# Kernel optimization log

Hardware: AMD Instinct MI355X
Metric: run time of the kernel (lower is better)

## Reference

```python
import jax, jax.numpy as jnp
import numpy as np

N_NODES = 50000
N_EDGES = 800000
H = 128
CHEM_DIM = 34   # 2 + 2*num_gdf
GEOM_DIM = 48   # 2*num_gdf + num_signatures
EPS = 1e-5


def _linear_params(key, d_in, d_out):
    kw, kb = jax.random.split(key)
    lim = 1.0 / np.sqrt(d_in)
    w = jax.random.uniform(kw, (d_in, d_out), jnp.float32, -lim, lim)
    b = jax.random.uniform(kb, (d_out,), jnp.float32, -lim, lim)
    return w, b


def setup_inputs() -> dict:
    key = jax.random.key(0)
    ks = jax.random.split(key, 16)
    inp = {
        'chem_feats': jax.random.normal(ks[0], (N_EDGES, CHEM_DIM), jnp.float32),
        'geom_feats': jax.random.normal(ks[1], (N_NODES, GEOM_DIM), jnp.float32),
        'nbr_vids': jax.random.randint(ks[2], (N_EDGES,), 0, N_NODES, jnp.int32),
    }
    # chem_mlp: Linear(34,128) -> BN(128) -> SiLU -> Linear(128,256) -> BN(256)
    inp['w_c1'], inp['b_c1'] = _linear_params(ks[3], CHEM_DIM, H)
    inp['g_c1'], inp['be_c1'] = jnp.ones((H,), jnp.float32), jnp.zeros((H,), jnp.float32)
    inp['w_c2'], inp['b_c2'] = _linear_params(ks[4], H, 2 * H)
    inp['g_c2'], inp['be_c2'] = jnp.ones((2 * H,), jnp.float32), jnp.zeros((2 * H,), jnp.float32)
    # geom_mlp: Linear(48,64) -> BN(64) -> SiLU -> Linear(64,64) -> BN(64)
    inp['w_g1'], inp['b_g1'] = _linear_params(ks[5], GEOM_DIM, H // 2)
    inp['g_g1'], inp['be_g1'] = jnp.ones((H // 2,), jnp.float32), jnp.zeros((H // 2,), jnp.float32)
    inp['w_g2'], inp['b_g2'] = _linear_params(ks[6], H // 2, H // 2)
    inp['g_g2'], inp['be_g2'] = jnp.ones((H // 2,), jnp.float32), jnp.zeros((H // 2,), jnp.float32)
    # feat_mlp: Linear(192,128) -> BN(128) -> SiLU -> Linear(128,128) -> BN(128)
    inp['w_f1'], inp['b_f1'] = _linear_params(ks[7], H + H // 2, H)
    inp['g_f1'], inp['be_f1'] = jnp.ones((H,), jnp.float32), jnp.zeros((H,), jnp.float32)
    inp['w_f2'], inp['b_f2'] = _linear_params(ks[8], H, H)
    inp['g_f2'], inp['be_f2'] = jnp.ones((H,), jnp.float32), jnp.zeros((H,), jnp.float32)
    return inp


def _bn(x, gamma, beta):
    # BatchNorm1d with batch statistics (training-mode normalization; dropout = identity at eval)
    m = jnp.mean(x, axis=0)
    v = jnp.var(x, axis=0)
    return gamma * (x - m) * jax.lax.rsqrt(v + EPS) + beta


def reference(chem_feats, geom_feats, nbr_vids,
              w_c1, b_c1, g_c1, be_c1, w_c2, b_c2, g_c2, be_c2,
              w_g1, b_g1, g_g1, be_g1, w_g2, b_g2, g_g2, be_g2,
              w_f1, b_f1, g_f1, be_f1, w_f2, b_f2, g_f2, be_f2):
    # chem branch: per-edge MLP
    h = _bn(chem_feats @ w_c1 + b_c1, g_c1, be_c1)
    h = jax.nn.silu(h)
    h = _bn(h @ w_c2 + b_c2, g_c2, be_c2)            # [E, 2H]
    nbr_filter, nbr_core = jnp.split(h, 2, axis=-1)
    h_chem = jax.nn.sigmoid(nbr_filter) * jax.nn.softplus(nbr_core)  # [E, H]
    # scatter-sum per-edge features into node bins
    h_chem = jax.ops.segment_sum(h_chem, nbr_vids, num_segments=N_NODES)  # [N, H]
    # geom branch: per-node MLP
    hg = _bn(geom_feats @ w_g1 + b_g1, g_g1, be_g1)
    hg = jax.nn.silu(hg)
    h_geom = _bn(hg @ w_g2 + b_g2, g_g2, be_g2)      # [N, H/2]
    # fuse
    hf = jnp.concatenate((h_chem, h_geom), axis=-1)  # [N, 3H/2]
    hf = _bn(hf @ w_f1 + b_f1, g_f1, be_f1)
    hf = jax.nn.silu(hf)
    h_out = _bn(hf @ w_f2 + b_f2, g_f2, be_f2)       # [N, H]
    return h_out
```

## Files before the change

### kernel.cpp

```cpp
#include <hip/hip_runtime.h>
#include <hip/hip_bf16.h>
#include <cmath>

#define E_EDGES 800000
#define N_NODES 50000
#define BN_EPS 1e-5f

typedef __attribute__((ext_vector_type(8))) short short8;
typedef __attribute__((ext_vector_type(4))) float float4v;
typedef unsigned short ushort_t;

#define MFMA16(a, b, c) __builtin_amdgcn_mfma_f32_16x16x32_bf16((a), (b), (c), 0, 0, 0)

#define OFF_GX 0
#define OFF_GH 2304
#define OFF_A1 23040
#define OFF_C1 23168
#define OFF_A2 23296
#define OFF_C2 23552
#define OFF_GS1SUM 23808
#define OFF_GS1SQ 23872
#define OFF_GS2SUM 23936
#define OFF_GS2SQ 24000
#define OFF_FS1SUM 24064
#define OFF_FS1SQ 24192
#define OFF_FS2SUM 24320
#define OFF_FS2SQ 24448
#define OFF_NODE 24576
#define OFF_TG2 (OFF_NODE + N_NODES * 128)
#define OFF_TF1 (OFF_TG2 + N_NODES * 64)
#define OFF_TF2 OFF_NODE
#define OFF_W1T (OFF_TF1 + N_NODES * 128)
#define OFF_W2T (OFF_W1T + 4096)

__device__ __forceinline__ float frcp_(float x) { return __builtin_amdgcn_rcpf(x); }
__device__ __forceinline__ float sigmoid_(float x) { return frcp_(1.0f + __expf(-x)); }
__device__ __forceinline__ float softplus_(float x) {
  return (x > 20.0f) ? x : __logf(1.0f + __expf(x));
}
__device__ __forceinline__ float silu_(float x) { return x * frcp_(1.0f + __expf(-x)); }

__device__ __forceinline__ ushort_t f2bf(float f) {
  __hip_bfloat16 h = __float2bfloat16(f);
  return *(ushort_t*)&h;
}
__device__ __forceinline__ float bf2f(ushort_t u) {
  return __uint_as_float(((unsigned)u) << 16);
}

__device__ __forceinline__ void load_xfrag(const float* __restrict__ chem, int e, int qd,
                                           short8* x0, short8* x1) {
  const float* xe = chem + e * 34;
  float2 p0 = *(const float2*)(xe + 8 * qd);
  float2 p1 = *(const float2*)(xe + 8 * qd + 2);
  float2 p2 = *(const float2*)(xe + 8 * qd + 4);
  float2 p3 = *(const float2*)(xe + 8 * qd + 6);
  short8 a;
  a[0] = (short)f2bf(p0.x); a[1] = (short)f2bf(p0.y);
  a[2] = (short)f2bf(p1.x); a[3] = (short)f2bf(p1.y);
  a[4] = (short)f2bf(p2.x); a[5] = (short)f2bf(p2.y);
  a[6] = (short)f2bf(p3.x); a[7] = (short)f2bf(p3.y);
  *x0 = a;
  short8 b = (short8){0, 0, 0, 0, 0, 0, 0, 0};
  if (qd == 0) {
    float2 pt = *(const float2*)(xe + 32);
    b[0] = (short)f2bf(pt.x); b[1] = (short)f2bf(pt.y);
  }
  *x1 = b;
}

__global__ __launch_bounds__(256) void k_prep(const float* __restrict__ w1,
                                              const float* __restrict__ w2,
                                              float* __restrict__ ws) {
  ushort_t* w1t = (ushort_t*)(ws + OFF_W1T);
  ushort_t* w2t = (ushort_t*)(ws + OFF_W2T);
  int idx = blockIdx.x * 256 + threadIdx.x;
  if (idx < 128 * 64) {
    int c = idx >> 6, k = idx & 63;
    float v = (k < 34) ? w1[k * 128 + c] : 0.0f;
    w1t[idx] = f2bf(v);
  }
  int j = idx - 128 * 64;
  if (j >= 0 && j < 256 * 128) {
    int c = j >> 7, k = j & 127;
    w2t[j] = f2bf(w2[k * 256 + c]);
  }
}

__global__ __launch_bounds__(256) void k_xstats(const float* __restrict__ chem,
                                                float* __restrict__ ws) {
  __shared__ __align__(16) ushort_t xT[2][48 * 72];
  const int t = threadIdx.x, wv = t >> 6, ln = t & 63, r15 = ln & 15, qd = ln >> 4;
  for (int i = t; i < 2 * 14 * 72; i += 256) {
    int b = i / (14 * 72), j = i % (14 * 72);
    int rr = j / 72, e = j % 72;
    xT[b][(34 + rr) * 72 + e] = (rr == 0 && e < 64) ? f2bf(1.0f) : (ushort_t)0;
  }
  float4v g0 = {0, 0, 0, 0}, g1 = {0, 0, 0, 0};
#pragma unroll 2
  for (int it = 0; it < 10; ++it) {
    const int st = blockIdx.x * 10 + it;
    const int buf = it & 1;
    for (int i = t; i < 64 * 34; i += 256) {
      int e = i / 34, k = i - e * 34;
      xT[buf][k * 72 + e] = f2bf(chem[st * 2176 + i]);
    }
    __syncthreads();
    const ushort_t* xb = &xT[buf][0];
#pragma unroll
    for (int ks = 0; ks < 2; ++ks) {
      const ushort_t* xk = xb + ks * 32 + 8 * qd;
      short8 f0 = *(const short8*)&xk[(0 + r15) * 72];
      short8 f1 = *(const short8*)&xk[(16 + r15) * 72];
      short8 f2v = *(const short8*)&xk[(32 + r15) * 72];
      if (wv == 0) { g0 = MFMA16(f0, f0, g0); g1 = MFMA16(f0, f1, g1); }
      else if (wv == 1) { g0 = MFMA16(f0, f2v, g0); g1 = MFMA16(f1, f1, g1); }
      else if (wv == 2) { g0 = MFMA16(f1, f2v, g0); }
      else { g0 = MFMA16(f2v, f2v, g0); }
    }
  }
  float* GX = ws + OFF_GX;
  int ti0, tj0, ti1 = -1, tj1 = -1;
  if (wv == 0) { ti0 = 0; tj0 = 0; ti1 = 0; tj1 = 1; }
  else if (wv == 1) { ti0 = 0; tj0 = 2; ti1 = 1; tj1 = 1; }
  else if (wv == 2) { ti0 = 1; tj0 = 2; }
  else { ti0 = 2; tj0 = 2; }
#pragma unroll
  for (int r = 0; r < 4; ++r)
    atomicAdd(&GX[(16 * ti0 + 4 * qd + r) * 48 + 16 * tj0 + r15], g0[r]);
  if (ti1 >= 0)
#pragma unroll
    for (int r = 0; r < 4; ++r)
      atomicAdd(&GX[(16 * ti1 + 4 * qd + r) * 48 + 16 * tj1 + r15], g1[r]);
}

__global__ __launch_bounds__(64) void k_bn1(const float* __restrict__ b1,
                                            const float* __restrict__ g1,
                                            const float* __restrict__ be1,
                                            float* __restrict__ ws) {
  const int c = blockIdx.x, i = threadIdx.x;
  __shared__ float wc[34];
  const ushort_t* w1t = (const ushort_t*)(ws + OFF_W1T);
  const float* GX = ws + OFF_GX;
  if (i < 34) wc[i] = bf2f(w1t[c * 64 + i]);
  __syncthreads();
  float p = 0.0f, ps = 0.0f;
  if (i < 34) {
    float gi = 0.0f;
    for (int j = 0; j < 34; ++j) {
      int a = i, b = j;
      if ((a >> 4) > (b >> 4)) { int tt = a; a = b; b = tt; }
      gi += GX[a * 48 + b] * wc[j];
    }
    p = wc[i] * gi;
    ps = wc[i] * GX[i * 48 + 34];
  }
#pragma unroll
  for (int off = 1; off < 64; off <<= 1) {
    p += __shfl_xor(p, off);
    ps += __shfl_xor(ps, off);
  }
  if (i == 0) {
    const float E = (float)E_EDGES;
    float bc = b1[c];
    float sum = ps + E * bc;
    float sq = p + 2.0f * bc * ps + E * bc * bc;
    float m = sum / E, v = sq / E - m * m;
    float a = g1[c] * rsqrtf(v + BN_EPS);
    ws[OFF_A1 + c] = a;
    ws[OFF_C1 + c] = a * (bc - m) + be1[c];
  }
}

template <int TJA, int TJB>
__device__ __forceinline__ void ghstep(const ushort_t* hk, int r15, float4v (&g)[11]) {
  short8 f[TJB + 1];
#pragma unroll
  for (int i = 0; i <= TJB; ++i) f[i] = *(const short8*)&hk[(16 * i + r15) * 72];
  short8 f8 = *(const short8*)&hk[(128 + r15) * 72];
  int s = 0;
#pragma unroll
  for (int ti = 0; ti <= TJA; ++ti) { g[s] = MFMA16(f[ti], f[TJA], g[s]); ++s; }
  g[s] = MFMA16(f8, f[TJA], g[s]); ++s;
#pragma unroll
  for (int ti = 0; ti <= TJB; ++ti) { g[s] = MFMA16(f[ti], f[TJB], g[s]); ++s; }
  g[s] = MFMA16(f8, f[TJB], g[s]);
}

__device__ __forceinline__ void ghtile(float* GH, int ti, int tj, int r15, int qd,
                                       const float4v v) {
#pragma unroll
  for (int r = 0; r < 4; ++r)
    atomicAdd(&GH[(16 * ti + 4 * qd + r) * 144 + 16 * tj + r15], v[r]);
}

template <int TJA, int TJB>
__device__ __forceinline__ void ghflush(float* GH, int r15, int qd, const float4v (&g)[11]) {
  int s = 0;
#pragma unroll
  for (int ti = 0; ti <= TJA; ++ti) { ghtile(GH, ti, TJA, r15, qd, g[s]); ++s; }
  ghtile(GH, 8, TJA, r15, qd, g[s]); ++s;
#pragma unroll
  for (int ti = 0; ti <= TJB; ++ti) { ghtile(GH, ti, TJB, r15, qd, g[s]); ++s; }
  ghtile(GH, 8, TJB, r15, qd, g[s]);
}

__global__ __launch_bounds__(256) void k_h(const float* __restrict__ chem,
                                           float* __restrict__ ws) {
  __shared__ __align__(16) ushort_t hT[2][144 * 72];
  const int t = threadIdx.x, wv = t >> 6, ln = t & 63, r15 = ln & 15, qd = ln >> 4;
  const ushort_t* w1t = (const ushort_t*)(ws + OFF_W1T);
  for (int i = t; i < 2 * 16 * 72; i += 256) {
    int b = i / (16 * 72), j = i % (16 * 72);
    int rr = j / 72, e = j % 72;
    hT[b][(128 + rr) * 72 + e] = (rr == 0 && e < 64) ? f2bf(1.0f) : (ushort_t)0;
  }
  float a1c[2], c1c[2];
#pragma unroll
  for (int cf = 0; cf < 2; ++cf) {
    int col = 32 * wv + 16 * cf + r15;
    a1c[cf] = ws[OFF_A1 + col];
    c1c[cf] = ws[OFF_C1 + col];
  }
  float4v gacc[11];
#pragma unroll
  for (int s = 0; s < 11; ++s) gacc[s] = (float4v){0, 0, 0, 0};

#pragma unroll 2
  for (int it = 0; it < 10; ++it) {
    const int st = blockIdx.x * 10 + it;
    const int buf = it & 1;
    const int e_base = st * 64;
    short8 xa0[4], xa1[4];
#pragma unroll
    for (int rb = 0; rb < 4; ++rb)
      load_xfrag(chem, e_base + 16 * rb + r15, qd, &xa0[rb], &xa1[rb]);
#pragma unroll
    for (int cf = 0; cf < 2; ++cf) {
      const int col = 32 * wv + 16 * cf + r15;
      short8 wb0 = *(const short8*)&w1t[col * 64 + 8 * qd];
      short8 wb1 = *(const short8*)&w1t[col * 64 + 32 + 8 * qd];
#pragma unroll
      for (int rb = 0; rb < 4; ++rb) {
        float4v acc = (float4v){0, 0, 0, 0};
        acc = MFMA16(xa0[rb], wb0, acc);
        acc = MFMA16(xa1[rb], wb1, acc);
        unsigned long long pk = 0;
#pragma unroll
        for (int r = 0; r < 4; ++r) {
          float hv = silu_(fmaf(a1c[cf], acc[r], c1c[cf]));
          pk |= ((unsigned long long)f2bf(hv)) << (16 * r);
        }
        *(unsigned long long*)&hT[buf][col * 72 + 16 * rb + 4 * qd] = pk;
      }
    }
    __syncthreads();
    const ushort_t* hb = &hT[buf][0];
#pragma unroll
    for (int ks = 0; ks < 2; ++ks) {
      const ushort_t* hk = hb + ks * 32 + 8 * qd;
      if (wv == 0) ghstep<0, 7>(hk, r15, gacc);
      else if (wv == 1) ghstep<1, 6>(hk, r15, gacc);
      else if (wv == 2) ghstep<2, 5>(hk, r15, gacc);
      else ghstep<3, 4>(hk, r15, gacc);
    }
  }
  float* GH = ws + OFF_GH;
  if (wv == 0) ghflush<0, 7>(GH, r15, qd, gacc);
  else if (wv == 1) ghflush<1, 6>(GH, r15, qd, gacc);
  else if (wv == 2) ghflush<2, 5>(GH, r15, qd, gacc);
  else ghflush<3, 4>(GH, r15, qd, gacc);
}

__global__ __launch_bounds__(128) void k_bn2(const float* __restrict__ b2,
                                             const float* __restrict__ g2,
                                             const float* __restrict__ be2,
                                             float* __restrict__ ws) {
  const int c = blockIdx.x, i = threadIdx.x;
  __shared__ float wcol[128];
  __shared__ float redQ[2], redS[2];
  const ushort_t* w2t = (const ushort_t*)(ws + OFF_W2T);
  const float* GH = ws + OFF_GH;
  wcol[i] = bf2f(w2t[c * 128 + i]);
  __syncthreads();
  float wi = wcol[i];
  float gi = 0.0f;
  for (int j = 0; j < 128; ++j) {
    int a = i, b = j;
    if ((a >> 4) > (b >> 4)) { int tt = a; a = b; b = tt; }
    gi += GH[a * 144 + b] * wcol[j];
  }
  float p = wi * gi;
  float ps = wi * GH[128 * 144 + i];
#pragma unroll
  for (int off = 1; off < 64; off <<= 1) {
    p += __shfl_xor(p, off);
    ps += __shfl_xor(ps, off);
  }
  const int wv = i >> 6, ln = i & 63;
  if (ln == 0) { redQ[wv] = p; redS[wv] = ps; }
  __syncthreads();
  if (i == 0) {
    float q = redQ[0] + redQ[1], s = redS[0] + redS[1];
    const float E = (float)E_EDGES;
    float bc = b2[c];
    float sum = s + E * bc;
    float sq = q + 2.0f * bc * s + E * bc * bc;
    float m = sum / E, v = sq / E - m * m;
    float a = g2[c] * rsqrtf(v + BN_EPS);
    ws[OFF_A2 + c] = a;
    ws[OFF_C2 + c] = a * (bc - m) + be2[c];
  }
}

__global__ __launch_bounds__(256) void k_scatter(const float* __restrict__ chem,
                                                 const int* __restrict__ vids,
                                                 float* __restrict__ ws) {
  __shared__ __align__(16) ushort_t hS[2][64 * 136];
  const int t = threadIdx.x, wv = t >> 6, ln = t & 63, r15 = ln & 15, qd = ln >> 4;
  const ushort_t* w1t = (const ushort_t*)(ws + OFF_W1T);
  const ushort_t* w2t = (const ushort_t*)(ws + OFF_W2T);
  float* node = ws + OFF_NODE;
  float a1c[2], c1c[2], aF2[2], cF2[2], aC2[2], cC2[2];
#pragma unroll
  for (int cf = 0; cf < 2; ++cf) {
    int col = 32 * wv + 16 * cf + r15;
    a1c[cf] = ws[OFF_A1 + col];
    c1c[cf] = ws[OFF_C1 + col];
    aF2[cf] = ws[OFF_A2 + col];
    cF2[cf] = ws[OFF_C2 + col];
    aC2[cf] = ws[OFF_A2 + 128 + col];
    cC2[cf] = ws[OFF_C2 + 128 + col];
  }
#pragma unroll 2
  for (int it = 0; it < 8; ++it) {
    const int st = blockIdx.x * 8 + it;
    if (st >= 12500) break;
    const int buf = it & 1;
    const int e_base = st * 64;
    const int myvid = vids[e_base + ln];
    short8 xa0[4], xa1[4];
#pragma unroll
    for (int rb = 0; rb < 4; ++rb)
      load_xfrag(chem, e_base + 16 * rb + r15, qd, &xa0[rb], &xa1[rb]);
#pragma unroll
    for (int cf = 0; cf < 2; ++cf) {
      const int col = 32 * wv + 16 * cf + r15;
      short8 wb0 = *(const short8*)&w1t[col * 64 + 8 * qd];
      short8 wb1 = *(const short8*)&w1t[col * 64 + 32 + 8 * qd];
#pragma unroll
      for (int rb = 0; rb < 4; ++rb) {
        float4v acc = (float4v){0, 0, 0, 0};
        acc = MFMA16(xa0[rb], wb0, acc);
        acc = MFMA16(xa1[rb], wb1, acc);
#pragma unroll
        for (int r = 0; r < 4; ++r) {
          float hv = silu_(fmaf(a1c[cf], acc[r], c1c[cf]));
          hS[buf][(16 * rb + 4 * qd + r) * 136 + col] = f2bf(hv);
        }
      }
    }
    __syncthreads();
    const ushort_t* hb = &hS[buf][0];
#pragma unroll
    for (int cf = 0; cf < 2; ++cf) {
      const int colF = 32 * wv + 16 * cf + r15;
      float4v accF[4], accC[4];
#pragma unroll
      for (int rb = 0; rb < 4; ++rb) {
        accF[rb] = (float4v){0, 0, 0, 0};
        accC[rb] = (float4v){0, 0, 0, 0};
      }
#pragma unroll
      for (int ks = 0; ks < 4; ++ks) {
        short8 bF = *(const short8*)&w2t[colF * 128 + ks * 32 + 8 * qd];
        short8 bC = *(const short8*)&w2t[(128 + colF) * 128 + ks * 32 + 8 * qd];
#pragma unroll
        for (int rb = 0; rb < 4; ++rb) {
          short8 hf = *(const short8*)&hb[(16 * rb + r15) * 136 + ks * 32 + 8 * qd];
          accF[rb] = MFMA16(hf, bF, accF[rb]);
          accC[rb] = MFMA16(hf, bC, accC[rb]);
        }
      }
#pragma unroll
      for (int rb = 0; rb < 4; ++rb)
#pragma unroll
        for (int r = 0; r < 4; ++r) {
          float F = fmaf(aF2[cf], accF[rb][r], cF2[cf]);
          float Co = fmaf(aC2[cf], accC[rb][r], cC2[cf]);
          float gv = sigmoid_(F) * softplus_(Co);
          int vid = __shfl(myvid, 16 * rb + 4 * qd + r);
          atomicAdd(node + (size_t)vid * 128 + colF, gv);
        }
    }
  }
}

__global__ __launch_bounds__(256) void k_geom_stats1(const float* __restrict__ geom,
                                                     const float* __restrict__ wg1,
                                                     const float* __restrict__ bg1,
                                                     float* __restrict__ ws) {
  __shared__ float ssum[64], ssq[64];
  const int t = threadIdx.x, lane = t & 63, w = t >> 6;
  if (t < 64) { ssum[t] = 0.0f; ssq[t] = 0.0f; }
  __syncthreads();
  const float bcol = bg1[lane];
  const int nb = blockIdx.x * 16 + w * 4;
  float x[4], acc[4];
#pragma unroll
  for (int u = 0; u < 4; u++) {
    x[u] = (lane < 48) ? geom[(nb + u) * 48 + lane] : 0.0f;
    acc[u] = bcol;
  }
#pragma unroll 16
  for (int k = 0; k < 48; k++) {
    float wvv = wg1[k * 64 + lane];
#pragma unroll
    for (int u = 0; u < 4; u++) acc[u] = fmaf(__shfl(x[u], k), wvv, acc[u]);
  }
  float bs = 0.0f, bq = 0.0f;
#pragma unroll
  for (int u = 0; u < 4; u++) { bs += acc[u]; bq += acc[u] * acc[u]; }
  atomicAdd(&ssum[lane], bs);
  atomicAdd(&ssq[lane], bq);
  __syncthreads();
  if (t < 64) {
    atomicAdd(ws + OFF_GS1SUM + t, ssum[t]);
    atomicAdd(ws + OFF_GS1SQ + t, ssq[t]);
  }
}

__global__ __launch_bounds__(256) void k_geom_main(
    const float* __restrict__ geom, const float* __restrict__ wg1,
    const float* __restrict__ bg1, const float* __restrict__ gg1,
    const float* __restrict__ beg1, const float* __restrict__ wg2,
    const float* __restrict__ bg2, float* __restrict__ ws) {
  __shared__ float ssum[64], ssq[64];
  const int t = threadIdx.x, lane = t & 63, w = t >> 6;
  if (t < 64) { ssum[t] = 0.0f; ssq[t] = 0.0f; }
  const float invN = 1.0f / (float)N_NODES;
  float s1 = ws[OFF_GS1SUM + lane], q1 = ws[OFF_GS1SQ + lane];
  float m1 = s1 * invN, v1 = q1 * invN - m1 * m1;
  float a1 = gg1[lane] * rsqrtf(v1 + BN_EPS);
  float c1 = beg1[lane] - a1 * m1;
  const float bcol = bg1[lane], b2col = bg2[lane];
  __syncthreads();
  const int nb = blockIdx.x * 16 + w * 4;
  float x[4], tg1[4], hg[4], acc[4];
#pragma unroll
  for (int u = 0; u < 4; u++) {
    x[u] = (lane < 48) ? geom[(nb + u) * 48 + lane] : 0.0f;
    tg1[u] = bcol;
  }
#pragma unroll 16
  for (int k = 0; k < 48; k++) {
    float wvv = wg1[k * 64 + lane];
#pragma unroll
    for (int u = 0; u < 4; u++) tg1[u] = fmaf(__shfl(x[u], k), wvv, tg1[u]);
  }
#pragma unroll
  for (int u = 0; u < 4; u++) {
    hg[u] = silu_(fmaf(a1, tg1[u], c1));
    acc[u] = b2col;
  }
#pragma unroll 16
  for (int k = 0; k < 64; k++) {
    float wvv = wg2[k * 64 + lane];
#pragma unroll
    for (int u = 0; u < 4; u++) acc[u] = fmaf(__shfl(hg[u], k), wvv, acc[u]);
  }
  float bs = 0.0f, bq = 0.0f;
#pragma unroll
  for (int u = 0; u < 4; u++) {
    ws[OFF_TG2 + (nb + u) * 64 + lane] = acc[u];
    bs += acc[u]; bq += acc[u] * acc[u];
  }
  atomicAdd(&ssum[lane], bs);
  atomicAdd(&ssq[lane], bq);
  __syncthreads();
  if (t < 64) {
    atomicAdd(ws + OFF_GS2SUM + t, ssum[t]);
    atomicAdd(ws + OFF_GS2SQ + t, ssq[t]);
  }
}

__global__ __launch_bounds__(256) void k_fuse1(const float* __restrict__ wf1,
                                               const float* __restrict__ bf1,
                                               const float* __restrict__ gg2,
                                               const float* __restrict__ beg2,
                                               float* __restrict__ ws) {
  __shared__ float ssum[128], ssq[128];
  const int t = threadIdx.x, lane = t & 63, w = t >> 6;
  if (t < 128) { ssum[t] = 0.0f; ssq[t] = 0.0f; }
  const float invN = 1.0f / (float)N_NODES;
  float s2 = ws[OFF_GS2SUM + lane], q2 = ws[OFF_GS2SQ + lane];
  float mg = s2 * invN, vg = q2 * invN - mg * mg;
  float ag = gg2[lane] * rsqrtf(vg + BN_EPS);
  float cg_ = beg2[lane] - ag * mg;
  const float bA = bf1[lane], bB = bf1[64 + lane];
  __syncthreads();
  const int nb = blockIdx.x * 16 + w * 4;
  float xa[4], xb[4], xg[4], acc1[4], acc2[4];
#pragma unroll
  for (int u = 0; u < 4; u++) {
    int n = nb + u;
    xa[u] = ws[OFF_NODE + n * 128 + lane];
    xb[u] = ws[OFF_NODE + n * 128 + 64 + lane];
    xg[u] = fmaf(ag, ws[OFF_TG2 + n * 64 + lane], cg_);
    acc1[u] = bA; acc2[u] = bB;
  }
#pragma unroll 16
  for (int k = 0; k < 64; k++) {
    float w1v = wf1[k * 128 + lane], w2v = wf1[k * 128 + 64 + lane];
#pragma unroll
    for (int u = 0; u < 4; u++) {
      float xk = __shfl(xa[u], k);
      acc1[u] = fmaf(xk, w1v, acc1[u]);
      acc2[u] = fmaf(xk, w2v, acc2[u]);
    }
  }
#pragma unroll 16
  for (int k = 0; k < 64; k++) {
    float w1v = wf1[(64 + k) * 128 + lane], w2v = wf1[(64 + k) * 128 + 64 + lane];
#pragma unroll
    for (int u = 0; u < 4; u++) {
      float xk = __shfl(xb[u], k);
      acc1[u] = fmaf(xk, w1v, acc1[u]);
      acc2[u] = fmaf(xk, w2v, acc2[u]);
    }
  }
#pragma unroll 16
  for (int k = 0; k < 64; k++) {
    float w1v = wf1[(128 + k) * 128 + lane], w2v = wf1[(128 + k) * 128 + 64 + lane];
#pragma unroll
    for (int u = 0; u < 4; u++) {
      float xk = __shfl(xg[u], k);
      acc1[u] = fmaf(xk, w1v, acc1[u]);
      acc2[u] = fmaf(xk, w2v, acc2[u]);
    }
  }
  float sA = 0, qA = 0, sB = 0, qB = 0;
#pragma unroll
  for (int u = 0; u < 4; u++) {
    int n = nb + u;
    ws[OFF_TF1 + n * 128 + lane] = acc1[u];
    ws[OFF_TF1 + n * 128 + 64 + lane] = acc2[u];
    sA += acc1[u]; qA += acc1[u] * acc1[u];
    sB += acc2[u]; qB += acc2[u] * acc2[u];
  }
  atomicAdd(&ssum[lane], sA); atomicAdd(&ssq[lane], qA);
  atomicAdd(&ssum[64 + lane], sB); atomicAdd(&ssq[64 + lane], qB);
  __syncthreads();
  if (t < 128) {
    atomicAdd(ws + OFF_FS1SUM + t, ssum[t]);
    atomicAdd(ws + OFF_FS1SQ + t, ssq[t]);
  }
}

__global__ __launch_bounds__(256) void k_fuse2(const float* __restrict__ wf2,
                                               const float* __restrict__ bf2,
                                               const float* __restrict__ gf1,
                                               const float* __restrict__ bef1,
                                               float* __restrict__ ws) {
  __shared__ float ssum[128], ssq[128];
  const int t = threadIdx.x, lane = t & 63, w = t >> 6;
  if (t < 128) { ssum[t] = 0.0f; ssq[t] = 0.0f; }
  const float invN = 1.0f / (float)N_NODES;
  float sA_ = ws[OFF_FS1SUM + lane], qA_ = ws[OFF_FS1SQ + lane];
  float mA = sA_ * invN, vA = qA_ * invN - mA * mA;
  float aA = gf1[lane] * rsqrtf(vA + BN_EPS);
  float cA = bef1[lane] - aA * mA;
  float sB_ = ws[OFF_FS1SUM + 64 + lane], qB_ = ws[OFF_FS1SQ + 64 + lane];
  float mB = sB_ * invN, vB = qB_ * invN - mB * mB;
  float aB = gf1[64 + lane] * rsqrtf(vB + BN_EPS);
  float cB = bef1[64 + lane] - aB * mB;
  const float b1c = bf2[lane], b2c = bf2[64 + lane];
  __syncthreads();
  const int nb = blockIdx.x * 16 + w * 4;
  float ha[4], hb[4], acc1[4], acc2[4];
#pragma unroll
  for (int u = 0; u < 4; u++) {
    int n = nb + u;
    ha[u] = silu_(fmaf(aA, ws[OFF_TF1 + n * 128 + lane], cA));
    hb[u] = silu_(fmaf(aB, ws[OFF_TF1 + n * 128 + 64 + lane], cB));
    acc1[u] = b1c; acc2[u] = b2c;
  }
#pragma unroll 16
  for (int k = 0; k < 64; k++) {
    float w1v = wf2[k * 128 + lane], w2v = wf2[k * 128 + 64 + lane];
#pragma unroll
    for (int u = 0; u < 4; u++) {
      float xk = __shfl(ha[u], k);
      acc1[u] = fmaf(xk, w1v, acc1[u]);
      acc2[u] = fmaf(xk, w2v, acc2[u]);
    }
  }
#pragma unroll 16
  for (int k = 0; k < 64; k++) {
    float w1v = wf2[(64 + k) * 128 + lane], w2v = wf2[(64 + k) * 128 + 64 + lane];
#pragma unroll
    for (int u = 0; u < 4; u++) {
      float xk = __shfl(hb[u], k);
      acc1[u] = fmaf(xk, w1v, acc1[u]);
      acc2[u] = fmaf(xk, w2v, acc2[u]);
    }
  }
  float sA = 0, qA = 0, sB = 0, qB = 0;
#pragma unroll
  for (int u = 0; u < 4; u++) {
    int n = nb + u;
    ws[OFF_TF2 + n * 128 + lane] = acc1[u];
    ws[OFF_TF2 + n * 128 + 64 + lane] = acc2[u];
    sA += acc1[u]; qA += acc1[u] * acc1[u];
    sB += acc2[u]; qB += acc2[u] * acc2[u];
  }
  atomicAdd(&ssum[lane], sA); atomicAdd(&ssq[lane], qA);
  atomicAdd(&ssum[64 + lane], sB); atomicAdd(&ssq[64 + lane], qB);
  __syncthreads();
  if (t < 128) {
    atomicAdd(ws + OFF_FS2SUM + t, ssum[t]);
    atomicAdd(ws + OFF_FS2SQ + t, ssq[t]);
  }
}

__global__ __launch_bounds__(256) void k_final(const float* __restrict__ gf2,
                                               const float* __restrict__ bef2,
                                               const float* __restrict__ ws,
                                               float* __restrict__ out) {
  const int idx = blockIdx.x * 256 + threadIdx.x;
  const int base = idx * 4;
  if (base >= N_NODES * 128) return;
  const float invN = 1.0f / (float)N_NODES;
  const int c0 = base & 127;
  float4 v = *(const float4*)(ws + OFF_TF2 + base);
  float vv[4] = {v.x, v.y, v.z, v.w}, r[4];
#pragma unroll
  for (int j = 0; j < 4; j++) {
    int c = c0 + j;
    float s = ws[OFF_FS2SUM + c], q = ws[OFF_FS2SQ + c];
    float m = s * invN, var = q * invN - m * m;
    float a = gf2[c] * rsqrtf(var + BN_EPS);
    r[j] = fmaf(a, vv[j] - m, bef2[c]);
  }
  *(float4*)(out + base) = make_float4(r[0], r[1], r[2], r[3]);
}

extern "C" void kernel_launch(void* const* d_in, const int* in_sizes, int n_in,
                              void* d_out, int out_size, void* d_ws, size_t ws_size,
                              hipStream_t stream) {
  const float* chem = (const float*)d_in[0];
  const float* geom = (const float*)d_in[1];
  const int* vids = (const int*)d_in[2];
  const float* w_c1 = (const float*)d_in[3];  const float* b_c1 = (const float*)d_in[4];
  const float* g_c1 = (const float*)d_in[5];  const float* be_c1 = (const float*)d_in[6];
  const float* w_c2 = (const float*)d_in[7];  const float* b_c2 = (const float*)d_in[8];
  const float* g_c2 = (const float*)d_in[9];  const float* be_c2 = (const float*)d_in[10];
  const float* w_g1 = (const float*)d_in[11]; const float* b_g1 = (const float*)d_in[12];
  const float* g_g1 = (const float*)d_in[13]; const float* be_g1 = (const float*)d_in[14];
  const float* w_g2 = (const float*)d_in[15]; const float* b_g2 = (const float*)d_in[16];
  const float* g_g2 = (const float*)d_in[17]; const float* be_g2 = (const float*)d_in[18];
  const float* w_f1 = (const float*)d_in[19]; const float* b_f1 = (const float*)d_in[20];
  const float* g_f1 = (const float*)d_in[21]; const float* be_f1 = (const float*)d_in[22];
  const float* w_f2 = (const float*)d_in[23]; const float* b_f2 = (const float*)d_in[24];
  const float* g_f2 = (const float*)d_in[25]; const float* be_f2 = (const float*)d_in[26];
  float* ws = (float*)d_ws;
  float* out = (float*)d_out;

  hipMemsetAsync(d_ws, 0, (size_t)(OFF_NODE + N_NODES * 128) * sizeof(float), stream);

  k_prep<<<dim3(160), dim3(256), 0, stream>>>(w_c1, w_c2, ws);
  k_xstats<<<dim3(1250), dim3(256), 0, stream>>>(chem, ws);
  k_bn1<<<dim3(128), dim3(64), 0, stream>>>(b_c1, g_c1, be_c1, ws);
  k_h<<<dim3(1250), dim3(256), 0, stream>>>(chem, ws);
  k_bn2<<<dim3(256), dim3(128), 0, stream>>>(b_c2, g_c2, be_c2, ws);
  k_scatter<<<dim3(1563), dim3(256), 0, stream>>>(chem, vids, ws);
  k_geom_stats1<<<dim3(3125), dim3(256), 0, stream>>>(geom, w_g1, b_g1, ws);
  k_geom_main<<<dim3(3125), dim3(256), 0, stream>>>(geom, w_g1, b_g1, g_g1, be_g1, w_g2, b_g2, ws);
  k_fuse1<<<dim3(3125), dim3(256), 0, stream>>>(w_f1, b_f1, g_g2, be_g2, ws);
  k_fuse2<<<dim3(3125), dim3(256), 0, stream>>>(w_f2, b_f2, g_f1, be_f1, ws);
  k_final<<<dim3(6250), dim3(256), 0, stream>>>(g_f2, be_f2, ws, out);
}
```

Before: 1.195 ms.

## Sort edges by node via counting sort and segment-reduce before atomics

Adds a histogram, two-level prefix scan and fill pass that build a node-sorted edge permutation. The scatter kernel then gathers chem rows in that order and stages the gated outputs in shared memory. It run-length reduces consecutive equal node ids before each atomicAdd, aiming to cut the roughly 100M float atomics. In exchange it adds four small kernels with their own int atomics, an indirect row gather, an extra barrier, and drops the double-buffered shared tile. With about 16 edges per node, each 32-row half-tile run should collapse many atomics.

Result: no change. 1.173 ms (-1.9%).

```diff
diff --git a/kernel.cpp b/kernel.cpp
--- a/kernel.cpp
+++ b/kernel.cpp
@@ -32,6 +32,12 @@
 #define OFF_TF2 OFF_NODE
 #define OFF_W1T (OFF_TF1 + N_NODES * 128)
 #define OFF_W2T (OFF_W1T + 4096)
+#define OFF_BASEI (OFF_W2T + 16384)
+#define OFF_BTOT (OFF_BASEI + 50176)
+#define OFF_CNT (OFF_BTOT + 256)
+#define OFF_CUR (OFF_CNT + 50176)
+#define OFF_SIDX (OFF_CUR + 50176)
+#define OFF_VIDS (OFF_SIDX + E_EDGES)
 
 __device__ __forceinline__ float frcp_(float x) { return __builtin_amdgcn_rcpf(x); }
 __device__ __forceinline__ float sigmoid_(float x) { return frcp_(1.0f + __expf(-x)); }
@@ -87,6 +93,74 @@
   }
 }
 
+__global__ __launch_bounds__(256) void k_hist(const int* __restrict__ vids,
+                                              float* __restrict__ ws) {
+  const int e = blockIdx.x * 256 + threadIdx.x;
+  int* cnt = (int*)(ws + OFF_CNT);
+  if (e < E_EDGES) atomicAdd(&cnt[vids[e]], 1);
+}
+
+__global__ __launch_bounds__(256) void k_scan1(float* __restrict__ ws) {
+  const int* cnt = (const int*)(ws + OFF_CNT);
+  int* base = (int*)(ws + OFF_BASEI);
+  int* btot = (int*)(ws + OFF_BTOT);
+  const int t = threadIdx.x, b = blockIdx.x, i = b * 256 + t;
+  const int lane = t & 63, w = t >> 6;
+  int c = (i < N_NODES) ? cnt[i] : 0;
+  int s = c;
+#pragma unroll
+  for (int o = 1; o < 64; o <<= 1) {
+    int y = __shfl_up(s, o);
+    if (lane >= o) s += y;
+  }
+  __shared__ int wsum[4];
+  if (lane == 63) wsum[w] = s;
+  __syncthreads();
+  int add = 0;
+#pragma unroll
+  for (int k = 0; k < 4; ++k)
+    if (k < w) add += wsum[k];
+  base[i] = s + add - c;
+  if (t == 255) btot[b] = s + add;
+}
+
+__global__ __launch_bounds__(256) void k_scan2(float* __restrict__ ws) {
+  int* btot = (int*)(ws + OFF_BTOT);
+  const int t = threadIdx.x;
+  const int lane = t & 63, w = t >> 6;
+  int c = (t < 196) ? btot[t] : 0;
+  int s = c;
+#pragma unroll
+  for (int o = 1; o < 64; o <<= 1) {
+    int y = __shfl_up(s, o);
+    if (lane >= o) s += y;
+  }
+  __shared__ int wsum[4];
+  if (lane == 63) wsum[w] = s;
+  __syncthreads();
+  int add = 0;
+#pragma unroll
+  for (int k = 0; k < 4; ++k)
+    if (k < w) add += wsum[k];
+  if (t < 196) btot[t] = s + add - c;
+}
+
+__global__ __launch_bounds__(256) void k_fill(const int* __restrict__ vids,
+                                              float* __restrict__ ws) {
+  const int e = blockIdx.x * 256 + threadIdx.x;
+  const int* base = (const int*)(ws + OFF_BASEI);
+  const int* btot = (const int*)(ws + OFF_BTOT);
+  int* cur = (int*)(ws + OFF_CUR);
+  int* sidx = (int*)(ws + OFF_SIDX);
+  int* vsrt = (int*)(ws + OFF_VIDS);
+  if (e < E_EDGES) {
+    int v = vids[e];
+    int pos = base[v] + btot[v >> 8] + atomicAdd(&cur[v], 1);
+    sidx[pos] = e;
+    vsrt[pos] = v;
+  }
+}
+
 __global__ __launch_bounds__(256) void k_xstats(const float* __restrict__ chem,
                                                 float* __restrict__ ws) {
   __shared__ __align__(16) ushort_t xT[2][48 * 72];
@@ -314,12 +388,15 @@
 }
 
 __global__ __launch_bounds__(256) void k_scatter(const float* __restrict__ chem,
-                                                 const int* __restrict__ vids,
                                                  float* __restrict__ ws) {
-  __shared__ __align__(16) ushort_t hS[2][64 * 136];
+  __shared__ __align__(16) ushort_t hS[64 * 136];
+  __shared__ __align__(16) float gS[64 * 133];
+  __shared__ int vS[64];
   const int t = threadIdx.x, wv = t >> 6, ln = t & 63, r15 = ln & 15, qd = ln >> 4;
   const ushort_t* w1t = (const ushort_t*)(ws + OFF_W1T);
   const ushort_t* w2t = (const ushort_t*)(ws + OFF_W2T);
+  const int* sidx = (const int*)(ws + OFF_SIDX);
+  const int* vsrt = (const int*)(ws + OFF_VIDS);
   float* node = ws + OFF_NODE;
   float a1c[2], c1c[2], aF2[2], cF2[2], aC2[2], cC2[2];
 #pragma unroll
@@ -332,17 +409,18 @@
     aC2[cf] = ws[OFF_A2 + 128 + col];
     cC2[cf] = ws[OFF_C2 + 128 + col];
   }
-#pragma unroll 2
   for (int it = 0; it < 8; ++it) {
     const int st = blockIdx.x * 8 + it;
     if (st >= 12500) break;
-    const int buf = it & 1;
     const int e_base = st * 64;
-    const int myvid = vids[e_base + ln];
+    const int myeid = sidx[e_base + ln];
+    const int myvid = vsrt[e_base + ln];
     short8 xa0[4], xa1[4];
 #pragma unroll
-    for (int rb = 0; rb < 4; ++rb)
-      load_xfrag(chem, e_base + 16 * rb + r15, qd, &xa0[rb], &xa1[rb]);
+    for (int rb = 0; rb < 4; ++rb) {
+      int er = __shfl(myeid, 16 * rb + r15);
+      load_xfrag(chem, er, qd, &xa0[rb], &xa1[rb]);
+    }
 #pragma unroll
     for (int cf = 0; cf < 2; ++cf) {
       const int col = 32 * wv + 16 * cf + r15;
@@ -356,12 +434,12 @@
 #pragma unroll
         for (int r = 0; r < 4; ++r) {
           float hv = silu_(fmaf(a1c[cf], acc[r], c1c[cf]));
-          hS[buf][(16 * rb + 4 * qd + r) * 136 + col] = f2bf(hv);
+          hS[(16 * rb + 4 * qd + r) * 136 + col] = f2bf(hv);
         }
       }
     }
     __syncthreads();
-    const ushort_t* hb = &hS[buf][0];
+    if (t < 64) vS[t] = myvid;
 #pragma unroll
     for (int cf = 0; cf < 2; ++cf) {
       const int colF = 32 * wv + 16 * cf + r15;
@@ -377,7 +455,7 @@
         short8 bC = *(const short8*)&w2t[(128 + colF) * 128 + ks * 32 + 8 * qd];
 #pragma unroll
         for (int rb = 0; rb < 4; ++rb) {
-          short8 hf = *(const short8*)&hb[(16 * rb + r15) * 136 + ks * 32 + 8 * qd];
+          short8 hf = *(const short8*)&hS[(16 * rb + r15) * 136 + ks * 32 + 8 * qd];
           accF[rb] = MFMA16(hf, bF, accF[rb]);
           accC[rb] = MFMA16(hf, bC, accC[rb]);
         }
@@ -388,10 +466,27 @@
         for (int r = 0; r < 4; ++r) {
           float F = fmaf(aF2[cf], accF[rb][r], cF2[cf]);
           float Co = fmaf(aC2[cf], accC[rb][r], cC2[cf]);
-          float gv = sigmoid_(F) * softplus_(Co);
-          int vid = __shfl(myvid, 16 * rb + 4 * qd + r);
-          atomicAdd(node + (size_t)vid * 128 + colF, gv);
+          gS[(16 * rb + 4 * qd + r) * 133 + colF] = sigmoid_(F) * softplus_(Co);
         }
+    }
+    __syncthreads();
+    {
+      const int c = t & 127, half = t >> 7;
+      const float* g = &gS[(32 * half) * 133 + c];
+      const int* vv = &vS[32 * half];
+      float acc = g[0];
+      int vcur = vv[0];
+      for (int r = 1; r < 32; ++r) {
+        int v = vv[r];
+        float x = g[r * 133];
+        if (v != vcur) {
+          atomicAdd(node + (size_t)vcur * 128 + c, acc);
+          acc = 0.0f;
+          vcur = v;
+        }
+        acc += x;
+      }
+      atomicAdd(node + (size_t)vcur * 128 + c, acc);
     }
   }
 }
@@ -667,13 +762,18 @@
   float* out = (float*)d_out;
 
   hipMemsetAsync(d_ws, 0, (size_t)(OFF_NODE + N_NODES * 128) * sizeof(float), stream);
+  hipMemsetAsync((void*)(ws + OFF_CNT), 0, (size_t)(2 * 50176) * sizeof(int), stream);
 
   k_prep<<<dim3(160), dim3(256), 0, stream>>>(w_c1, w_c2, ws);
+  k_hist<<<dim3(3125), dim3(256), 0, stream>>>(vids, ws);
+  k_scan1<<<dim3(196), dim3(256), 0, stream>>>(ws);
+  k_scan2<<<dim3(1), dim3(256), 0, stream>>>(ws);
+  k_fill<<<dim3(3125), dim3(256), 0, stream>>>(vids, ws);
   k_xstats<<<dim3(1250), dim3(256), 0, stream>>>(chem, ws);
   k_bn1<<<dim3(128), dim3(64), 0, stream>>>(b_c1, g_c1, be_c1, ws);
   k_h<<<dim3(1250), dim3(256), 0, stream>>>(chem, ws);
   k_bn2<<<dim3(256), dim3(128), 0, stream>>>(b_c2, g_c2, be_c2, ws);
-  k_scatter<<<dim3(1563), dim3(256), 0, stream>>>(chem, vids, ws);
+  k_scatter<<<dim3(1563), dim3(256), 0, stream>>>(chem, ws);
   k_geom_stats1<<<dim3(3125), dim3(256), 0, stream>>>(geom, w_g1, b_g1, ws);
   k_geom_main<<<dim3(3125), dim3(256), 0, stream>>>(geom, w_g1, b_g1, g_g1, be_g1, w_g2, b_g2, ws);
   k_fuse1<<<dim3(3125), dim3(256), 0, stream>>>(w_f1, b_f1, g_g2, be_g2, ws);
```
